# Optimization experiments

Measured on AMD Instinct MI355X. Metric: run time of the kernel, lower is better.

Reference implementation:

```python
import jax, jax.numpy as jnp
import numpy as np

B, HID, NH = 2048, 512, 8
HD = HID // NH


def _slstm(x, W, b, R, h, c):
    # gates = W_gates(x) + R_gates(h); chunk order i,f,g,o
    g = x @ W.T + b + h @ R.T
    i, f, gg, o = jnp.split(g, 4, axis=1)
    c_new = jax.nn.sigmoid(f) * c + jnp.exp(i) * jnp.tanh(gg)
    return jax.nn.sigmoid(o) * jnp.tanh(c_new)


def _mlstm(x, Wq, bq, Wk, bk, Wv, bv, igw, igb, fgw, fgb, lng, lnb):
    Bsz = x.shape[0]
    q = (x @ Wq.T + bq).reshape(Bsz, NH, HD)
    k = (x @ Wk.T + bk).reshape(Bsz, NH, HD)
    v = (x @ Wv.T + bv).reshape(Bsz, NH, HD)
    i = jnp.exp(x @ igw.T + igb)            # [B,H] input gate (exponential)
    f = jax.nn.sigmoid(x @ fgw.T + fgb)     # [B,H]; multiplies zero init state -> drops out
    # initial state (C, n, m) is zeros, so C_new = i * (v k^T), n_new = i * v, m_new = i
    C = i[:, :, None, None] * (v[..., :, None] * k[..., None, :])  # [B,H,hd,hd]
    n = i[:, :, None] * v                                          # [B,H,hd]
    m = i                                                          # [B,H]
    num = jnp.einsum('bhij,bhj->bhi', C, q)
    den = jnp.einsum('bhi,bhi->bh', n, q) + m + 1e-6
    h = (num / den[..., None]).reshape(Bsz, HID)
    mu = h.mean(-1, keepdims=True)
    var = ((h - mu) ** 2).mean(-1, keepdims=True)
    return (h - mu) / jnp.sqrt(var + 1e-5) * lng + lnb


def setup_inputs() -> dict:
    key = jax.random.key(0)
    ks = iter(jax.random.split(key, 64))
    rn = lambda shape, s: jax.random.normal(next(ks), shape, dtype=jnp.float32) * s
    inp = {
        'V': jax.random.normal(next(ks), (B, 1), dtype=jnp.float32),
        't': jax.random.uniform(next(ks), (B, 1), dtype=jnp.float32),
        'ip_w': rn((HID, 2), 0.1), 'ip_b': rn((HID,), 0.02),
        'op_w': rn((1, HID), 0.05), 'op_b': rn((1,), 0.02),
    }
    for p in ('s0', 's2'):
        inp[p + '_W'] = rn((4 * HID, HID), 0.05)
        inp[p + '_b'] = rn((4 * HID,), 0.05)
        inp[p + '_R'] = rn((4 * HID, HID), 0.05)
    for p in ('m1', 'm3'):
        for nm in ('Wq', 'Wk', 'Wv'):
            inp[p + '_' + nm] = rn((HID, HID), 0.05)
        for nm in ('bq', 'bk', 'bv'):
            inp[p + '_' + nm] = rn((HID,), 0.02)
        inp[p + '_igw'] = rn((NH, HID), 0.05)
        inp[p + '_igb'] = rn((NH,), 0.1)
        inp[p + '_fgw'] = rn((NH, HID), 0.05)
        inp[p + '_fgb'] = jnp.linspace(3.0, 6.0, NH, dtype=jnp.float32)
        inp[p + '_lng'] = jnp.ones((HID,), dtype=jnp.float32)
        inp[p + '_lnb'] = jnp.zeros((HID,), dtype=jnp.float32)
    return inp


def reference(V, t, ip_w, ip_b, op_w, op_b,
              s0_W, s0_b, s0_R, s2_W, s2_b, s2_R,
              m1_Wq, m1_Wk, m1_Wv, m1_bq, m1_bk, m1_bv,
              m1_igw, m1_igb, m1_fgw, m1_fgb, m1_lng, m1_lnb,
              m3_Wq, m3_Wk, m3_Wv, m3_bq, m3_bk, m3_bv,
              m3_igw, m3_igb, m3_fgw, m3_fgb, m3_lng, m3_lnb):
    x = jnp.concatenate([V, t], axis=1)           # [B,2]
    h = x @ ip_w.T + ip_b                         # [B,HID]
    z = jnp.zeros((h.shape[0], HID), h.dtype)
    h = _slstm(h, s0_W, s0_b, s0_R, z, z)         # layer 0: sLSTM
    h = _mlstm(h, m1_Wq, m1_bq, m1_Wk, m1_bk, m1_Wv, m1_bv,
               m1_igw, m1_igb, m1_fgw, m1_fgb, m1_lng, m1_lnb)  # layer 1: mLSTM
    h = _slstm(h, s2_W, s2_b, s2_R, z, z)         # layer 2: sLSTM
    h = _mlstm(h, m3_Wq, m3_bq, m3_Wk, m3_bk, m3_Wv, m3_bv,
               m3_igw, m3_igb, m3_fgw, m3_fgb, m3_lng, m3_lnb)  # layer 3: mLSTM
    return h @ op_w.T + op_b                      # I_pred [B,1]
```

## Files before the change

### kernel.cpp

```cpp
#include <hip/hip_runtime.h>
#include <hip/hip_bf16.h>

#define HID 512
#define BATCH 2048

typedef __bf16 bf16x8 __attribute__((ext_vector_type(8)));
typedef float f32x4 __attribute__((ext_vector_type(4)));
typedef float f32x16 __attribute__((ext_vector_type(16)));
typedef __hip_bfloat16 bf16;

__device__ inline unsigned short f2bf(float x) {
    bf16 h = __float2bfloat16(x);
    return __builtin_bit_cast(unsigned short, h);
}
__device__ inline float bf2f(unsigned short u) {
    return __bfloat162float(__builtin_bit_cast(bf16, u));
}

__device__ inline void gload16(const void* g, void* l) {
    __builtin_amdgcn_global_load_lds((const __attribute__((address_space(1))) void*)g,
                                     (__attribute__((address_space(3))) void*)l, 16, 0, 0);
}

struct CvtArgs { const float* src[7]; };

__global__ void k_prep(CvtArgs a, unsigned short* __restrict__ hi, unsigned short* __restrict__ lo,
                       const float* __restrict__ s0W, const float* __restrict__ s0b,
                       const float* __restrict__ ipw, const float* __restrict__ ipb,
                       float* __restrict__ uV, float* __restrict__ uT, float* __restrict__ uC) {
    const int bid = blockIdx.x;
    if (bid < 2560) {
        int idx4 = (bid * 256 + threadIdx.x) << 2;
        int seg, off; size_t dst;
        if (idx4 < 1048576) { seg = 0; off = idx4; dst = 1048576 + idx4; }
        else { int r = idx4 - 1048576; seg = 1 + (r >> 18); off = r & 262143; dst = 2097152 + r; }
        f32x4 w = *(const f32x4*)(a.src[seg] + off);
        ushort4 h, l;
        h.x = f2bf(w[0]); h.y = f2bf(w[1]); h.z = f2bf(w[2]); h.w = f2bf(w[3]);
        l.x = f2bf(w[0] - bf2f(h.x)); l.y = f2bf(w[1] - bf2f(h.y));
        l.z = f2bf(w[2] - bf2f(h.z)); l.w = f2bf(w[3] - bf2f(h.w));
        *(ushort4*)(hi + dst) = h;
        *(ushort4*)(lo + dst) = l;
    } else {
        const int w = threadIdx.x >> 6, lane = threadIdx.x & 63;
        const int r = (bid - 2560) * 4 + w;
        const int wr = r < 512 ? r : r + 512;
        const float* Wp = s0W + (size_t)wr * HID + lane * 8;
        f32x4 wa = *(const f32x4*)Wp, wb = *(const f32x4*)(Wp + 4);
        const float* pw = ipw + lane * 16;
        f32x4 e0 = *(const f32x4*)pw,       e1 = *(const f32x4*)(pw + 4);
        f32x4 e2 = *(const f32x4*)(pw + 8), e3 = *(const f32x4*)(pw + 12);
        f32x4 ba = *(const f32x4*)(ipb + lane * 8), bb = *(const f32x4*)(ipb + lane * 8 + 4);
        float s0 = wa[0]*e0[0] + wa[1]*e0[2] + wa[2]*e1[0] + wa[3]*e1[2]
                 + wb[0]*e2[0] + wb[1]*e2[2] + wb[2]*e3[0] + wb[3]*e3[2];
        float s1 = wa[0]*e0[1] + wa[1]*e0[3] + wa[2]*e1[1] + wa[3]*e1[3]
                 + wb[0]*e2[1] + wb[1]*e2[3] + wb[2]*e3[1] + wb[3]*e3[3];
        float s2 = wa[0]*ba[0] + wa[1]*ba[1] + wa[2]*ba[2] + wa[3]*ba[3]
                 + wb[0]*bb[0] + wb[1]*bb[1] + wb[2]*bb[2] + wb[3]*bb[3];
#pragma unroll
        for (int off = 32; off; off >>= 1) {
            s0 += __shfl_xor(s0, off); s1 += __shfl_xor(s1, off); s2 += __shfl_xor(s2, off);
        }
        if (lane == 0) { uV[r] = s0; uT[r] = s1; uC[r] = s2 + s0b[wr]; }
    }
}

__global__ void k_slstm0(const float* __restrict__ V, const float* __restrict__ t,
                         const float* __restrict__ uV, const float* __restrict__ uT,
                         const float* __restrict__ uC,
                         unsigned short* __restrict__ hhi, unsigned short* __restrict__ hlo) {
    int idx = blockIdx.x * blockDim.x + threadIdx.x;
    int b = idx >> 7, j4 = (idx & 127) << 2;
    float vv = V[b], tt = t[b];
    f32x4 gi = vv * *(const f32x4*)(uV + j4)        + tt * *(const f32x4*)(uT + j4)        + *(const f32x4*)(uC + j4);
    f32x4 gg = vv * *(const f32x4*)(uV + 512 + j4)  + tt * *(const f32x4*)(uT + 512 + j4)  + *(const f32x4*)(uC + 512 + j4);
    f32x4 go = vv * *(const f32x4*)(uV + 1024 + j4) + tt * *(const f32x4*)(uT + 1024 + j4) + *(const f32x4*)(uC + 1024 + j4);
    ushort4 h, l;
    float x[4];
#pragma unroll
    for (int u = 0; u < 4; ++u)
        x[u] = tanhf(expf(gi[u]) * tanhf(gg[u])) / (1.f + expf(-go[u]));
    h.x = f2bf(x[0]); h.y = f2bf(x[1]); h.z = f2bf(x[2]); h.w = f2bf(x[3]);
    l.x = f2bf(x[0] - bf2f(h.x)); l.y = f2bf(x[1] - bf2f(h.y));
    l.z = f2bf(x[2] - bf2f(h.z)); l.w = f2bf(x[3] - bf2f(h.w));
    size_t o = (size_t)b * HID + j4;
    *(ushort4*)(hhi + o) = h;
    *(ushort4*)(hlo + o) = l;
}

__global__ __launch_bounds__(512) void k_gemm(
    const bf16* __restrict__ Ahi, const bf16* __restrict__ Alo,
    const bf16* __restrict__ Wh0, const bf16* __restrict__ Wh1, const bf16* __restrict__ Wh2,
    const bf16* __restrict__ Wl0, const bf16* __restrict__ Wl1, const bf16* __restrict__ Wl2,
    float* __restrict__ C)
{
    __shared__ __align__(16) bf16 lds[5][8192];
    const int tid = threadIdx.x, w = tid >> 6, lane = tid & 63;

    const int bid = blockIdx.x;
    const int xcd = bid & 7, slot = bid >> 3;
    const int m0 = (xcd * 2 + slot / 12) * 128;
    const int n0 = (slot % 12) * 128;
    const int nseg = n0 >> 9, nloc = n0 & 511;
    const bf16* Wh = nseg == 0 ? Wh0 : (nseg == 1 ? Wh1 : Wh2);
    const bf16* Wl = nseg == 0 ? Wl0 : (nseg == 1 ? Wl1 : Wl2);

    auto src_of = [&](int c) -> const bf16* {
        const int m = c >> 2, rb = c & 3;
        const bf16* base = (m == 0) ? Ahi : (m == 1) ? Alo : (m == 2) ? Wh : Wl;
        const int rowbase = (m < 2) ? m0 : nloc;
        return base + (size_t)(rowbase + (rb << 5) + (lane & 31)) * HID + ((lane >> 5) << 3);
    };
    const int c0 = 2 * w;
    const bf16* sp0 = src_of(c0);
    const bf16* sp1 = src_of(c0 + 1);
    bf16* const d0 = &lds[0][0] + (c0 << 9) + (lane << 3);

    auto STAGE = [&](int t) {
        bf16* db = d0 + (t % 5) * 8192;
        gload16(sp0 + (t << 4), db);
        gload16(sp1 + (t << 4), db + 512);
    };

    const int wm = w >> 1, wn = w & 1;
    const int la = lane << 3;
    const int cA  = wm << 9;
    const int cAl = (4 + wm) << 9;
    const int cW0 = (8 + 2 * wn) << 9;
    const int cW1 = (9 + 2 * wn) << 9;
    const int cL0 = (12 + 2 * wn) << 9;
    const int cL1 = (13 + 2 * wn) << 9;
    f32x16 acc0 = {}, acc1 = {};

    STAGE(0); STAGE(1); STAGE(2); STAGE(3);
#pragma unroll
    for (int t = 0; t < 32; ++t) {
        if (t < 29)
            asm volatile("s_waitcnt vmcnt(6) lgkmcnt(0)\n\ts_barrier" ::: "memory");
        else if (t == 29)
            asm volatile("s_waitcnt vmcnt(4) lgkmcnt(0)\n\ts_barrier" ::: "memory");
        else if (t == 30)
            asm volatile("s_waitcnt vmcnt(2) lgkmcnt(0)\n\ts_barrier" ::: "memory");
        else
            asm volatile("s_waitcnt vmcnt(0) lgkmcnt(0)\n\ts_barrier" ::: "memory");
        if (t < 28) STAGE(t + 4);
        const bf16* lb = &lds[t % 5][0];
        bf16x8 ah  = *(const bf16x8*)(lb + cA  + la);
        bf16x8 al  = *(const bf16x8*)(lb + cAl + la);
        bf16x8 wh0 = *(const bf16x8*)(lb + cW0 + la);
        bf16x8 wh1 = *(const bf16x8*)(lb + cW1 + la);
        bf16x8 wl0 = *(const bf16x8*)(lb + cL0 + la);
        bf16x8 wl1 = *(const bf16x8*)(lb + cL1 + la);
        acc0 = __builtin_amdgcn_mfma_f32_32x32x16_bf16(ah, wh0, acc0, 0, 0, 0);
        acc1 = __builtin_amdgcn_mfma_f32_32x32x16_bf16(ah, wh1, acc1, 0, 0, 0);
        acc0 = __builtin_amdgcn_mfma_f32_32x32x16_bf16(al, wh0, acc0, 0, 0, 0);
        acc1 = __builtin_amdgcn_mfma_f32_32x32x16_bf16(al, wh1, acc1, 0, 0, 0);
        acc0 = __builtin_amdgcn_mfma_f32_32x32x16_bf16(ah, wl0, acc0, 0, 0, 0);
        acc1 = __builtin_amdgcn_mfma_f32_32x32x16_bf16(ah, wl1, acc1, 0, 0, 0);
    }

    const int rb4 = (lane >> 5) << 2;
#pragma unroll
    for (int f = 0; f < 2; ++f) {
        const f32x16& ac = f ? acc1 : acc0;
        const int col = n0 + ((2 * wn + f) << 5) + (lane & 31);
#pragma unroll
        for (int rr = 0; rr < 16; ++rr) {
            int row = m0 + (wm << 5) + (rr & 3) + ((rr >> 2) << 3) + rb4;
            C[(size_t)row * 1536 + col] = ac[rr];
        }
    }
}

__global__ void k_slstm_act(const float* __restrict__ g, const float* __restrict__ bp,
                            unsigned short* __restrict__ hhi, unsigned short* __restrict__ hlo) {
    int idx = blockIdx.x * blockDim.x + threadIdx.x;
    int b = idx >> 7, j4 = (idx & 127) << 2;
    const float* r0 = g + (size_t)b * 1536 + j4;
    f32x4 gi = *(const f32x4*)r0 + *(const f32x4*)(bp + j4);
    f32x4 gg = *(const f32x4*)(r0 + 512) + *(const f32x4*)(bp + 1024 + j4);
    f32x4 go = *(const f32x4*)(r0 + 1024) + *(const f32x4*)(bp + 1536 + j4);
    ushort4 h, l;
    float x[4];
#pragma unroll
    for (int u = 0; u < 4; ++u)
        x[u] = tanhf(expf(gi[u]) * tanhf(gg[u])) / (1.f + expf(-go[u]));
    h.x = f2bf(x[0]); h.y = f2bf(x[1]); h.z = f2bf(x[2]); h.w = f2bf(x[3]);
    l.x = f2bf(x[0] - bf2f(h.x)); l.y = f2bf(x[1] - bf2f(h.y));
    l.z = f2bf(x[2] - bf2f(h.z)); l.w = f2bf(x[3] - bf2f(h.w));
    size_t o = (size_t)b * HID + j4;
    *(ushort4*)(hhi + o) = h;
    *(ushort4*)(hlo + o) = l;
}

__global__ __launch_bounds__(512) void k_mlstm(
    const float* __restrict__ g0,
    const float* __restrict__ bq, const float* __restrict__ bk, const float* __restrict__ bv,
    const bf16* __restrict__ hinh, const bf16* __restrict__ hinl,
    const float* __restrict__ igw, const float* __restrict__ igb,
    const float* __restrict__ lng, const float* __restrict__ lnb,
    unsigned short* __restrict__ outh, unsigned short* __restrict__ outl,
    const float* __restrict__ opw, const float* __restrict__ opb, float* __restrict__ out)
{
    int b = blockIdx.x;
    int tid = threadIdx.x, head = tid >> 6, lane = tid & 63;

    const bf16*  hh = hinh + (size_t)b * HID;
    const bf16*  hl = hinl + (size_t)b * HID;
    const float* wrow = igw + head * HID;
    float s = 0.f;
#pragma unroll
    for (int k = 0; k < 8; ++k) {
        int p = lane + 64 * k;
        s += wrow[p] * (__bfloat162float(hh[p]) + __bfloat162float(hl[p]));
    }
#pragma unroll
    for (int off = 32; off; off >>= 1) s += __shfl_xor(s, off);
    float ig = expf(s + igb[head]);

    const float* r0 = g0 + (size_t)b * 1536;
    float q  = r0[tid] + bq[tid];
    float kk = r0[512 + tid] + bk[tid];
    float v  = r0[1024 + tid] + bv[tid];
    float kq = kk * q, vq = v * q;
#pragma unroll
    for (int off = 32; off; off >>= 1) { kq += __shfl_xor(kq, off); vq += __shfl_xor(vq, off); }
    float den = ig * (vq + 1.0f) + 1e-6f;
    float hv  = v * (ig * kq) / den;

    __shared__ float red[16];
    __shared__ float red2[8];
    float s1 = hv, s2 = hv * hv;
#pragma unroll
    for (int off = 32; off; off >>= 1) { s1 += __shfl_xor(s1, off); s2 += __shfl_xor(s2, off); }
    if (lane == 0) { red[head] = s1; red[8 + head] = s2; }
    __syncthreads();
    float t1 = 0.f, t2 = 0.f;
#pragma unroll
    for (int h2 = 0; h2 < 8; ++h2) { t1 += red[h2]; t2 += red[8 + h2]; }
    float mu  = t1 * (1.f / 512.f);
    float var = t2 * (1.f / 512.f) - mu * mu;
    float o = (hv - mu) * rsqrtf(var + 1e-5f) * lng[tid] + lnb[tid];

    if (out) {
        float po = o * opw[tid];
#pragma unroll
        for (int off = 32; off; off >>= 1) po += __shfl_xor(po, off);
        if (lane == 0) red2[head] = po;
        __syncthreads();
        if (tid == 0) {
            float tt = 0.f;
#pragma unroll
            for (int h2 = 0; h2 < 8; ++h2) tt += red2[h2];
            out[b] = tt + opb[0];
        }
    } else {
        unsigned short oh = f2bf(o);
        size_t p = (size_t)b * HID + tid;
        outh[p] = oh;
        outl[p] = f2bf(o - bf2f(oh));
    }
}

extern "C" void kernel_launch(void* const* d_in, const int* in_sizes, int n_in,
                              void* d_out, int out_size, void* d_ws, size_t ws_size,
                              hipStream_t stream) {
    const float* V    = (const float*)d_in[0];
    const float* t    = (const float*)d_in[1];
    const float* ip_w = (const float*)d_in[2];
    const float* ip_b = (const float*)d_in[3];
    const float* op_w = (const float*)d_in[4];
    const float* op_b = (const float*)d_in[5];
    const float* s0_W = (const float*)d_in[6];
    const float* s0_b = (const float*)d_in[7];
    const float* s2_W = (const float*)d_in[9];
    const float* s2_b = (const float*)d_in[10];
    const float* m1_Wq = (const float*)d_in[12];
    const float* m1_Wk = (const float*)d_in[13];
    const float* m1_Wv = (const float*)d_in[14];
    const float* m1_bq = (const float*)d_in[15];
    const float* m1_bk = (const float*)d_in[16];
    const float* m1_bv = (const float*)d_in[17];
    const float* m1_igw = (const float*)d_in[18];
    const float* m1_igb = (const float*)d_in[19];
    const float* m1_lng = (const float*)d_in[22];
    const float* m1_lnb = (const float*)d_in[23];
    const float* m3_Wq = (const float*)d_in[24];
    const float* m3_Wk = (const float*)d_in[25];
    const float* m3_Wv = (const float*)d_in[26];
    const float* m3_bq = (const float*)d_in[27];
    const float* m3_bk = (const float*)d_in[28];
    const float* m3_bv = (const float*)d_in[29];
    const float* m3_igw = (const float*)d_in[30];
    const float* m3_igb = (const float*)d_in[31];
    const float* m3_lng = (const float*)d_in[34];
    const float* m3_lnb = (const float*)d_in[35];

    char* ws = (char*)d_ws;
    bf16* whi  = (bf16*)ws;
    bf16* wlo  = (bf16*)(ws + 7340032);
    bf16* hAhi = (bf16*)(ws + 14680064);
    bf16* hAlo = (bf16*)(ws + 16777216);
    bf16* hBhi = (bf16*)(ws + 18874368);
    bf16* hBlo = (bf16*)(ws + 20971520);
    float* gq  = (float*)(ws + 23068672);
    float* uV  = (float*)(ws + 35651584);
    float* uT  = uV + 1536;
    float* uC  = uT + 1536;

    CvtArgs ca;
    ca.src[0] = s2_W;
    ca.src[1] = m1_Wq; ca.src[2] = m1_Wk; ca.src[3] = m1_Wv;
    ca.src[4] = m3_Wq; ca.src[5] = m3_Wk; ca.src[6] = m3_Wv;
    k_prep<<<2944, 256, 0, stream>>>(ca, (unsigned short*)whi, (unsigned short*)wlo,
                                     s0_W, s0_b, ip_w, ip_b, uV, uT, uC);

    k_slstm0<<<1024, 256, 0, stream>>>(V, t, uV, uT, uC,
                                       (unsigned short*)hBhi, (unsigned short*)hBlo);
    k_gemm<<<192, 512, 0, stream>>>(hBhi, hBlo,
        whi + 2097152, whi + 2359296, whi + 2621440,
        wlo + 2097152, wlo + 2359296, wlo + 2621440, gq);
    k_mlstm<<<BATCH, 512, 0, stream>>>(gq, m1_bq, m1_bk, m1_bv, hBhi, hBlo,
                                       m1_igw, m1_igb, m1_lng, m1_lnb,
                                       (unsigned short*)hAhi, (unsigned short*)hAlo,
                                       nullptr, nullptr, nullptr);
    k_gemm<<<192, 512, 0, stream>>>(hAhi, hAlo,
        whi + 1048576, whi + 1572864, whi + 1835008,
        wlo + 1048576, wlo + 1572864, wlo + 1835008, gq);
    k_slstm_act<<<1024, 256, 0, stream>>>(gq, s2_b, (unsigned short*)hBhi, (unsigned short*)hBlo);
    k_gemm<<<192, 512, 0, stream>>>(hBhi, hBlo,
        whi + 2883584, whi + 3145728, whi + 3407872,
        wlo + 2883584, wlo + 3145728, wlo + 3407872, gq);
    k_mlstm<<<BATCH, 512, 0, stream>>>(gq, m3_bq, m3_bk, m3_bv, hBhi, hBlo,
                                       m3_igw, m3_igb, m3_lng, m3_lnb,
                                       nullptr, nullptr,
                                       op_w, op_b, (float*)d_out);
}
```

Measured before the change: 101.5 us.

## Fuse first sLSTM activation into the following GEMM's A-operand generation

Removes the separate k_slstm0 kernel and computes the layer-0 sLSTM output on the fly inside a new GEMM kernel, writing the bf16 hi/lo split straight into LDS as the A tile. Only the blocks with the first N-tile also write the hidden state to global memory for the later residual use in mLSTM. This saves one launch and a global round trip of the A operand. In exchange, each of the 12 N-tile blocks per row recomputes the transcendentals, and the pipeline wait counts are changed per block role.

Measured after the change: 256.0 us. +152.2%, slower.

```diff
diff --git a/kernel.cpp b/kernel.cpp
--- a/kernel.cpp
+++ b/kernel.cpp
@@ -65,27 +65,138 @@
     }
 }
 
-__global__ void k_slstm0(const float* __restrict__ V, const float* __restrict__ t,
-                         const float* __restrict__ uV, const float* __restrict__ uT,
-                         const float* __restrict__ uC,
-                         unsigned short* __restrict__ hhi, unsigned short* __restrict__ hlo) {
-    int idx = blockIdx.x * blockDim.x + threadIdx.x;
-    int b = idx >> 7, j4 = (idx & 127) << 2;
-    float vv = V[b], tt = t[b];
-    f32x4 gi = vv * *(const f32x4*)(uV + j4)        + tt * *(const f32x4*)(uT + j4)        + *(const f32x4*)(uC + j4);
-    f32x4 gg = vv * *(const f32x4*)(uV + 512 + j4)  + tt * *(const f32x4*)(uT + 512 + j4)  + *(const f32x4*)(uC + 512 + j4);
-    f32x4 go = vv * *(const f32x4*)(uV + 1024 + j4) + tt * *(const f32x4*)(uT + 1024 + j4) + *(const f32x4*)(uC + 1024 + j4);
-    ushort4 h, l;
-    float x[4];
-#pragma unroll
-    for (int u = 0; u < 4; ++u)
-        x[u] = tanhf(expf(gi[u]) * tanhf(gg[u])) / (1.f + expf(-go[u]));
-    h.x = f2bf(x[0]); h.y = f2bf(x[1]); h.z = f2bf(x[2]); h.w = f2bf(x[3]);
-    l.x = f2bf(x[0] - bf2f(h.x)); l.y = f2bf(x[1] - bf2f(h.y));
-    l.z = f2bf(x[2] - bf2f(h.z)); l.w = f2bf(x[3] - bf2f(h.w));
-    size_t o = (size_t)b * HID + j4;
-    *(ushort4*)(hhi + o) = h;
-    *(ushort4*)(hlo + o) = l;
+__global__ __launch_bounds__(512) void k_gemm1(
+    const float* __restrict__ Vin, const float* __restrict__ Tin,
+    const float* __restrict__ uVg, const float* __restrict__ uTg, const float* __restrict__ uCg,
+    const bf16* __restrict__ Wh0, const bf16* __restrict__ Wh1, const bf16* __restrict__ Wh2,
+    const bf16* __restrict__ Wl0, const bf16* __restrict__ Wl1, const bf16* __restrict__ Wl2,
+    unsigned short* __restrict__ hBhi, unsigned short* __restrict__ hBlo,
+    float* __restrict__ C)
+{
+    __shared__ __align__(16) bf16 lds[5][8192];
+    __shared__ __align__(16) float ubuf[4608];
+    const int tid = threadIdx.x, w = tid >> 6, lane = tid & 63;
+
+    const int bid = blockIdx.x;
+    const int xcd = bid & 7, slot = bid >> 3;
+    const int m0 = (xcd * 2 + slot / 12) * 128;
+    const int n0 = (slot % 12) * 128;
+    const int nseg = n0 >> 9, nloc = n0 & 511;
+    const bf16* Wh = nseg == 0 ? Wh0 : (nseg == 1 ? Wh1 : Wh2);
+    const bf16* Wl = nseg == 0 ? Wl0 : (nseg == 1 ? Wl1 : Wl2);
+    const bool whb = (slot % 12) == 0;
+
+    for (int i = tid; i < 1536; i += 512) {
+        ubuf[i] = uVg[i];
+        ubuf[1536 + i] = uTg[i];
+        ubuf[3072 + i] = uCg[i];
+    }
+
+    const int cw = (w >= 4) ? 2 * w : 8;
+    auto wsrc = [&](int c) -> const bf16* {
+        const bf16* base = ((c >> 2) == 2) ? Wh : Wl;
+        return base + (size_t)(nloc + ((c & 3) << 5) + (lane & 31)) * HID + ((lane >> 5) << 3);
+    };
+    const bf16* sp0 = wsrc(cw);
+    const bf16* sp1 = wsrc(cw + 1);
+    bf16* const wdst = &lds[0][0] + (cw << 9) + (lane << 3);
+
+    const int rb = w & 3;
+    const int grow = m0 + (rb << 5) + (lane & 31);
+    const int kpart = ((w >> 2) << 3) + ((lane >> 5) << 2);
+    const float Vv = Vin[grow], Tv = Tin[grow];
+    const int aoff = ((lane & 31) << 4) + ((w >> 2) << 9) + ((lane >> 5) << 3);
+
+    auto AGEN = [&](int t) {
+        const int kk = (t << 4) + kpart;
+        f32x4 vi = *(const f32x4*)&ubuf[kk];
+        f32x4 ti = *(const f32x4*)&ubuf[1536 + kk];
+        f32x4 ci = *(const f32x4*)&ubuf[3072 + kk];
+        f32x4 vg = *(const f32x4*)&ubuf[512 + kk];
+        f32x4 tg = *(const f32x4*)&ubuf[2048 + kk];
+        f32x4 cg = *(const f32x4*)&ubuf[3584 + kk];
+        f32x4 vo = *(const f32x4*)&ubuf[1024 + kk];
+        f32x4 to = *(const f32x4*)&ubuf[2560 + kk];
+        f32x4 co = *(const f32x4*)&ubuf[4096 + kk];
+        ushort4 h4, l4;
+#pragma unroll
+        for (int j = 0; j < 4; ++j) {
+            float gi = Vv * vi[j] + Tv * ti[j] + ci[j];
+            float gg = Vv * vg[j] + Tv * tg[j] + cg[j];
+            float go = Vv * vo[j] + Tv * to[j] + co[j];
+            float x = tanhf(expf(gi) * tanhf(gg)) / (1.f + expf(-go));
+            unsigned short hh = f2bf(x);
+            unsigned short ll = f2bf(x - bf2f(hh));
+            if (j == 0) { h4.x = hh; l4.x = ll; }
+            else if (j == 1) { h4.y = hh; l4.y = ll; }
+            else if (j == 2) { h4.z = hh; l4.z = ll; }
+            else { h4.w = hh; l4.w = ll; }
+        }
+        char* lb = (char*)&lds[t % 5][0];
+        *(ushort4*)(lb + (rb << 10) + aoff) = h4;
+        *(ushort4*)(lb + ((4 + rb) << 10) + aoff) = l4;
+        if (whb) {
+            *(ushort4*)(hBhi + (size_t)grow * HID + kk) = h4;
+            *(ushort4*)(hBlo + (size_t)grow * HID + kk) = l4;
+        }
+    };
+    auto WSTAGE = [&](int t) {
+        if (w >= 4) {
+            bf16* db = wdst + (t % 5) * 8192;
+            gload16(sp0 + (t << 4), db);
+            gload16(sp1 + (t << 4), db + 512);
+        }
+    };
+
+    __syncthreads();
+    WSTAGE(0); AGEN(0); WSTAGE(1); AGEN(1); WSTAGE(2); AGEN(2); WSTAGE(3); AGEN(3);
+
+    const int wm = w >> 1, wn = w & 1;
+    const int la = lane << 3;
+    const int cA  = wm << 9;
+    const int cAl = (4 + wm) << 9;
+    const int cW0 = (8 + 2 * wn) << 9;
+    const int cW1 = (9 + 2 * wn) << 9;
+    const int cL0 = (12 + 2 * wn) << 9;
+    const int cL1 = (13 + 2 * wn) << 9;
+    f32x16 acc0 = {}, acc1 = {};
+
+#pragma unroll
+    for (int t = 0; t < 32; ++t) {
+        if (t < 28) {
+            if (whb) asm volatile("s_waitcnt vmcnt(14) lgkmcnt(0)" ::: "memory");
+            else     asm volatile("s_waitcnt vmcnt(6) lgkmcnt(0)" ::: "memory");
+        } else {
+            asm volatile("s_waitcnt vmcnt(0) lgkmcnt(0)" ::: "memory");
+        }
+        asm volatile("s_barrier" ::: "memory");
+        if (t < 28) { WSTAGE(t + 4); AGEN(t + 4); }
+        const bf16* lb = &lds[t % 5][0];
+        bf16x8 ah  = *(const bf16x8*)(lb + cA  + la);
+        bf16x8 al  = *(const bf16x8*)(lb + cAl + la);
+        bf16x8 wh0 = *(const bf16x8*)(lb + cW0 + la);
+        bf16x8 wh1 = *(const bf16x8*)(lb + cW1 + la);
+        bf16x8 wl0 = *(const bf16x8*)(lb + cL0 + la);
+        bf16x8 wl1 = *(const bf16x8*)(lb + cL1 + la);
+        acc0 = __builtin_amdgcn_mfma_f32_32x32x16_bf16(ah, wh0, acc0, 0, 0, 0);
+        acc1 = __builtin_amdgcn_mfma_f32_32x32x16_bf16(ah, wh1, acc1, 0, 0, 0);
+        acc0 = __builtin_amdgcn_mfma_f32_32x32x16_bf16(al, wh0, acc0, 0, 0, 0);
+        acc1 = __builtin_amdgcn_mfma_f32_32x32x16_bf16(al, wh1, acc1, 0, 0, 0);
+        acc0 = __builtin_amdgcn_mfma_f32_32x32x16_bf16(ah, wl0, acc0, 0, 0, 0);
+        acc1 = __builtin_amdgcn_mfma_f32_32x32x16_bf16(ah, wl1, acc1, 0, 0, 0);
+    }
+
+    const int rb4 = (lane >> 5) << 2;
+#pragma unroll
+    for (int f = 0; f < 2; ++f) {
+        const f32x16& ac = f ? acc1 : acc0;
+        const int col = n0 + ((2 * wn + f) << 5) + (lane & 31);
+#pragma unroll
+        for (int rr = 0; rr < 16; ++rr) {
+            int row = m0 + (wm << 5) + (rr & 3) + ((rr >> 2) << 3) + rb4;
+            C[(size_t)row * 1536 + col] = ac[rr];
+        }
+    }
 }
 
 __global__ __launch_bounds__(512) void k_gemm(
@@ -315,11 +426,10 @@
     k_prep<<<2944, 256, 0, stream>>>(ca, (unsigned short*)whi, (unsigned short*)wlo,
                                      s0_W, s0_b, ip_w, ip_b, uV, uT, uC);
 
-    k_slstm0<<<1024, 256, 0, stream>>>(V, t, uV, uT, uC,
-                                       (unsigned short*)hBhi, (unsigned short*)hBlo);
-    k_gemm<<<192, 512, 0, stream>>>(hBhi, hBlo,
+    k_gemm1<<<192, 512, 0, stream>>>(V, t, uV, uT, uC,
         whi + 2097152, whi + 2359296, whi + 2621440,
-        wlo + 2097152, wlo + 2359296, wlo + 2621440, gq);
+        wlo + 2097152, wlo + 2359296, wlo + 2621440,
+        (unsigned short*)hBhi, (unsigned short*)hBlo, gq);
     k_mlstm<<<BATCH, 512, 0, stream>>>(gq, m1_bq, m1_bk, m1_bv, hBhi, hBlo,
                                        m1_igw, m1_igb, m1_lng, m1_lnb,
                                        (unsigned short*)hAhi, (unsigned short*)hAlo,
```
